# Optimization experiments

Measured on AMD Instinct MI355X. Metric: run time of the kernel, lower is better.

The kernel has to match this reference:

```python
import jax, jax.numpy as jnp
import numpy as np

RATE = 2
KSIZE = 3          # patch size for similarity
KERNEL = 2 * RATE  # patch size for alpha scatter (4)
BN_EPS = 1e-5


def _extract_patches(x, k, s):
    """Mirror of GuidedCxtAtten.extract_patches: reflect-pad then unfold.
    x: [B,C,H,W] -> [B,Ho,Wo,C,k,k] with Ho=H//s, Wo=W//s."""
    left = (k - s + 1) // 2
    right = (k - s) // 2
    xp = jnp.pad(x, ((0, 0), (0, 0), (left, right), (left, right)), mode='reflect')
    Hp, Wp = xp.shape[2], xp.shape[3]
    Ho = (Hp - k) // s + 1
    Wo = (Wp - k) // s + 1
    ii = (jnp.arange(Ho) * s)[:, None] + jnp.arange(k)[None, :]   # [Ho,k]
    jj = (jnp.arange(Wo) * s)[:, None] + jnp.arange(k)[None, :]   # [Wo,k]
    p = xp[:, :, ii[:, :, None, None], jj[None, None, :, :]]      # [B,C,Ho,k,Wo,k]
    return p.transpose(0, 2, 4, 1, 3, 5)                          # [B,Ho,Wo,C,k,k]


def setup_inputs() -> dict:
    key = jax.random.key(0)
    ks = jax.random.split(key, 5)
    B, Cg, Ca, H, W = 4, 256, 128, 128, 128
    f = jax.random.normal(ks[0], (B, Cg, H, W), dtype=jnp.float32)
    alpha = jax.random.normal(ks[1], (B, Ca, H, W), dtype=jnp.float32)
    unknown = (jax.random.uniform(ks[2], (B, 1, H, W)) > 0.5).astype(jnp.float32)
    # guidance_conv: 1x1, Cg -> Cg//2, xavier-ish
    gc_w = jax.random.normal(ks[3], (Cg // 2, Cg), dtype=jnp.float32) * np.sqrt(2.0 / (Cg + Cg // 2))
    gc_b = jnp.zeros((Cg // 2,), dtype=jnp.float32)
    # W[0]: 1x1 conv Ca->Ca no bias; W[1]: BN with gamma=0.001, beta=0 per init
    w_w = jax.random.normal(ks[4], (Ca, Ca), dtype=jnp.float32) * np.sqrt(1.0 / Ca)
    bn_gamma = jnp.full((Ca,), 0.001, dtype=jnp.float32)
    bn_beta = jnp.zeros((Ca,), dtype=jnp.float32)
    return {"f": f, "alpha": alpha, "unknown": unknown, "gc_w": gc_w, "gc_b": gc_b,
            "w_w": w_w, "bn_gamma": bn_gamma, "bn_beta": bn_beta}


def _forward(f, alpha, unknown, gc_w, gc_b, w_w, bn_gamma, bn_beta):
    # guidance 1x1 conv
    fg = jnp.einsum('oi,bihw->bohw', gc_w, f) + gc_b[None, :, None, None]
    B, _, H, W = fg.shape
    Ca = alpha.shape[1]
    Hs, Ws = H // RATE, W // RATE
    L = Hs * Ws

    # alpha patches [B,L,Ca,4,4] (kernel=2*rate, stride=rate)
    alpha_w = _extract_patches(alpha, KERNEL, RATE).reshape(B, L, Ca, KERNEL, KERNEL)

    # nearest downsample by rate (torch nearest with scale 1/2 == strided pick)
    f_ds = fg[:, :, ::RATE, ::RATE]                # [B,Cg/2,Hs,Ws]
    unk_ds = unknown[:, :, ::RATE, ::RATE]         # [B,1,Hs,Ws]

    # similarity filter patches [B,L,C,3,3]
    w = _extract_patches(f_ds, KSIZE, 1).reshape(B, L, -1, KSIZE, KSIZE)

    # known/unknown softmax scales [B,2]
    u_mean = unk_ds.mean(axis=(2, 3))              # [B,1]
    k_mean = 1.0 - u_mean
    su = jnp.clip(jnp.sqrt(u_mean / k_mean), 0.1, 10.0)
    sk = jnp.clip(jnp.sqrt(k_mean / u_mean), 0.1, 10.0)
    softmax_scale = jnp.concatenate([su, sk], axis=1)

    # patch-mean of unknown mask -> binary patch mask [B,L]
    m = _extract_patches(unk_ds, KSIZE, 1).reshape(B, L, -1).mean(axis=2)
    mm = (m > 0.0).astype(fg.dtype)

    # l2-normalize filters per patch, then correlate against all positions.
    # Conv of reflect-padded f_ds with stride-1 3x3 patch filters == inner
    # product of normalized patches with the raw patches (same extraction).
    norm = jnp.sqrt(jnp.sum(w * w, axis=(2, 3, 4), keepdims=True))
    w_normed = w / jnp.maximum(norm, 1e-4)
    scores = jnp.einsum('bqcij,bpcij->bqp', w_normed, w)   # [B,L(q=patch),L(p=pos)]

    # known/unknown scaling per source patch q
    gate = jnp.where(mm > 0.0, su, sk)                      # [B,L]
    scores = scores * gate[:, :, None]

    # self-match suppression only for unknown patches (diagonal q == p)
    diag = jnp.arange(L)
    scores = scores.at[:, diag, diag].add(-10000.0 * mm)

    attn = jax.nn.softmax(scores, axis=1)                   # softmax over patches q

    # offsets (argmax patch per position, relative to center)
    idx = jnp.argmax(attn, axis=1)                          # [B,L]
    offsets = jnp.stack([idx // Ws, idx % Ws], axis=1).reshape(B, 2, Hs, Ws)
    offsets = offsets - jnp.array([Hs // 2, Ws // 2]).reshape(1, 2, 1, 1)

    # scatter alpha patches with attention weights: per-sample conv_transpose2d
    attn_map = attn.reshape(B, L, Hs, Ws)

    def ct(yi, wc):  # yi [L,Hs,Ws], wc [L,Ca,4,4]
        rhs = jnp.flip(wc, (2, 3)).transpose(1, 0, 2, 3)    # [Ca,L,4,4]
        pad = KERNEL - 1 - 1                                # torch padding=1
        out = jax.lax.conv_general_dilated(
            yi[None], rhs, window_strides=(1, 1),
            padding=[(pad, pad), (pad, pad)], lhs_dilation=(RATE, RATE),
            dimension_numbers=('NCHW', 'OIHW', 'NCHW'))
        return out[0]

    y = jax.vmap(ct)(attn_map, alpha_w) / 4.0               # [B,Ca,H,W]

    # W: 1x1 conv (no bias) + BatchNorm2d (training-mode batch stats)
    yw = jnp.einsum('oi,bihw->bohw', w_w, y)
    mean = yw.mean(axis=(0, 2, 3))
    var = yw.var(axis=(0, 2, 3))
    yn = (yw - mean[None, :, None, None]) * jax.lax.rsqrt(var + BN_EPS)[None, :, None, None]
    yn = yn * bn_gamma[None, :, None, None] + bn_beta[None, :, None, None]

    return yn + alpha, offsets, softmax_scale


def reference(f, alpha, unknown, gc_w, gc_b, w_w, bn_gamma, bn_beta):
    return _forward(f, alpha, unknown, gc_w, gc_b, w_w, bn_gamma, bn_beta)
```

## Files before the change

### kernel.cpp

```cpp
#include <hip/hip_runtime.h>
#include <math.h>

#define B 4
#define CG 256
#define CM 128
#define CA 128
#define H 128
#define W_ 128
#define HS 64
#define WS 64
#define L 4096
#define D1 1152
#define D2 2048
#define NPIX 65536
#define NT1 36
#define NT2 128

#define STP_F 8388608UL
#define WF_F  4718592UL
#define ZB_F  4194304UL
#define SLOT_F (STP_F + WF_F + ZB_F)

typedef unsigned short u16;
typedef __attribute__((ext_vector_type(8))) short short8v;
typedef __attribute__((ext_vector_type(4))) unsigned short u16x4;
typedef __attribute__((ext_vector_type(4))) float f32x4;

__device__ __forceinline__ float bf2f(u16 x) {
    union { unsigned int u; float f; } v; v.u = ((unsigned int)x) << 16; return v.f;
}
__device__ __forceinline__ u16 f2bf(float x) {
    union { float f; unsigned int u; } v; v.f = x;
    unsigned int r = (v.u + 0x7FFFu + ((v.u >> 16) & 1u)) >> 16;
    return (u16)r;
}
__device__ __forceinline__ void gll16(const void* g, void* l) {
    __builtin_amdgcn_global_load_lds((const __attribute__((address_space(1))) void*)g,
                                     (__attribute__((address_space(3))) void*)l, 16, 0, 0);
}
__device__ __forceinline__ int refl(int i, int n) {
    return i < 0 ? -i : (i >= n ? 2 * n - 2 - i : i);
}
__device__ __forceinline__ int swz(int row, int fq) {
    return row * 32 + ((fq ^ ((row >> 1) & 3)) * 8);
}

__device__ __forceinline__ void stage32(const u16* __restrict__ mat, int rowTile,
                                        int kt, u16* lds, int wid, int lane) {
#pragma unroll
    for (int c = 0; c < 2; ++c) {
        int off = c * 8192 + wid * 1024 + lane * 16;
        int row = off >> 6;
        int cb  = off & 63;
        const u16* g = mat + (size_t)(rowTile + row) * L + kt * 32
                     + ((cb ^ (((row >> 1) & 3) << 4)) >> 1);
        gll16(g, (char*)lds + c * 8192 + wid * 1024);
    }
}
__device__ __forceinline__ short8v rdfrag32(const u16* lds, int r, int fq) {
    return *(const short8v*)((const char*)lds + r * 64 + ((fq * 16) ^ (((r >> 1) & 3) << 4)));
}

__global__ __launch_bounds__(256) void k_conv_ds(const float* __restrict__ f,
                                                 const float* __restrict__ gw,
                                                 const float* __restrict__ gb,
                                                 float* __restrict__ fds,
                                                 float* __restrict__ ssq) {
    __shared__ float sf[CG * 64];
    __shared__ float part[4][64];
    int t = threadIdx.x;
    int hs = blockIdx.x, b = blockIdx.y;
    const float* fb = f + (size_t)b * CG * H * W_ + (2 * hs) * W_;
    for (int idx = t; idx < CG * 64; idx += 256) {
        int ci = idx >> 6, ws = idx & 63;
        sf[idx] = fb[(size_t)ci * H * W_ + 2 * ws];
    }
    __syncthreads();
    int ws = t & 63;
    int wave = __builtin_amdgcn_readfirstlane(t >> 6);
    const float* gwp = gw + (size_t)(wave * 32) * CG;
    float acc[32];
#pragma unroll
    for (int r = 0; r < 32; ++r) acc[r] = gb[wave * 32 + r];
    for (int ci = 0; ci < CG; ++ci) {
        float fv = sf[ci * 64 + ws];
#pragma unroll
        for (int r = 0; r < 32; ++r) acc[r] += gwp[r * CG + ci] * fv;
    }
    float sq = 0.f;
#pragma unroll
    for (int r = 0; r < 32; ++r) {
        int co = wave * 32 + r;
        fds[(((size_t)b * CM + co) * HS + hs) * WS + ws] = acc[r];
        sq += acc[r] * acc[r];
    }
    part[wave][ws] = sq;
    __syncthreads();
    if (t < 64)
        ssq[((size_t)b * HS + hs) * WS + t] =
            part[0][t] + part[1][t] + part[2][t] + part[3][t];
}

__global__ __launch_bounds__(256) void k_scale(const float* __restrict__ unk,
                                               float* __restrict__ suk,
                                               float* __restrict__ out2) {
    int b = blockIdx.x, t = threadIdx.x;
    __shared__ float red[256];
    float s = 0.f;
    for (int i = t; i < L; i += 256) {
        int hs = i >> 6, ws = i & 63;
        s += unk[(size_t)b * H * W_ + (2 * hs) * W_ + 2 * ws];
    }
    red[t] = s;
    __syncthreads();
    for (int o = 128; o > 0; o >>= 1) {
        if (t < o) red[t] += red[t + o];
        __syncthreads();
    }
    if (t == 0) {
        float u = red[0] / (float)L;
        float k = 1.0f - u;
        float su = sqrtf(u / k); su = fminf(fmaxf(su, 0.1f), 10.0f);
        float sk = sqrtf(k / u); sk = fminf(fmaxf(sk, 0.1f), 10.0f);
        suk[b * 2] = su; suk[b * 2 + 1] = sk;
        out2[b * 2] = su; out2[b * 2 + 1] = sk;
    }
}

__global__ __launch_bounds__(64) void k_gate(const float* __restrict__ unk,
                                             const float* __restrict__ ssq,
                                             const float* __restrict__ suk,
                                             float* __restrict__ g,
                                             float* __restrict__ dg) {
    int ws = threadIdx.x, hs = blockIdx.x, b = blockIdx.y;
    float sm = 0.f, sq = 0.f;
    for (int di = -1; di <= 1; ++di) {
        int rh = refl(hs + di, HS);
        for (int dj = -1; dj <= 1; ++dj) {
            int rw = refl(ws + dj, WS);
            sm += unk[(size_t)b * H * W_ + (2 * rh) * W_ + 2 * rw];
            sq += ssq[((size_t)b * HS + rh) * WS + rw];
        }
    }
    float mm   = (sm > 0.0f) ? 1.0f : 0.0f;
    float norm = sqrtf(sq);
    float gate = (mm > 0.0f) ? suk[2 * b] : suk[2 * b + 1];
    int q = hs * WS + ws;
    g[(size_t)b * L + q]  = gate / fmaxf(norm, 1e-4f);
    dg[(size_t)b * L + q] = -10000.0f * mm;
}

__global__ __launch_bounds__(256) void k_buildW(const float* __restrict__ fds,
                                                float* __restrict__ base, int b0) {
    int bz = blockIdx.z;
    int b  = b0 + bz;
    float* S   = base + (size_t)bz * SLOT_F;
    float* Wf  = S + STP_F;
    u16*   Whi = (u16*)(S + STP_F + WF_F);
    int ws = threadIdx.x;
    int c  = blockIdx.y * 4 + threadIdx.y;
    int hs = blockIdx.x;
    int q = hs * WS + ws;
    size_t bo = (size_t)q * D1 + c * 9;
    const float* src = fds + ((size_t)b * CM + c) * HS * WS;
#pragma unroll
    for (int i = 0; i < 3; ++i) {
        int rh = refl(hs + i - 1, HS);
#pragma unroll
        for (int j = 0; j < 3; ++j) {
            int rw = refl(ws + j - 1, WS);
            float v = src[rh * WS + rw];
            Wf[bo + i * 3 + j]  = v;
            Whi[bo + i * 3 + j] = f2bf(v);
        }
    }
}

__global__ __launch_bounds__(256) void k_gemm1(float* __restrict__ base,
                                               const float* __restrict__ g0,
                                               const float* __restrict__ dg0,
                                               int b0) {
    __shared__ u16 sA[3][128 * 32], sB[3][128 * 32];
    int bz = blockIdx.z;
    float* S = base + (size_t)bz * SLOT_F;
    u16* STP = (u16*)S;
    const u16* Whi = (const u16*)(S + STP_F + WF_F);
    const float* g  = g0  + (size_t)(b0 + bz) * L;
    const float* dg = dg0 + (size_t)(b0 + bz) * L;

    int tid = threadIdx.x;
    int wv = tid >> 6, lane = tid & 63;
    int t0 = blockIdx.x, I = 0;
    while (t0 >= 32 - I) { t0 -= 32 - I; ++I; }
    int J = I + t0;
    int pTile = I * 128, qTile = J * 128;
    int wp = (wv >> 1) * 64, wq = (wv & 1) * 64;
    int r0 = wv * 32;
    int lrow = lane >> 2;
    int csw = ((lane & 3) ^ ((lrow >> 1) & 3)) * 8;
    int fr = lane & 15, fq = lane >> 4;

    const u16* gArow = Whi + (size_t)(pTile + r0 + lrow) * D1 + csw;
    const u16* gBrow = Whi + (size_t)(qTile + r0 + lrow) * D1 + csw;

#define G1STAGE(kt, bf) do { \
    gll16(gArow + (kt) * 32, &sA[bf][r0 * 32]); \
    gll16(gArow + (kt) * 32 + (size_t)16 * D1, &sA[bf][(r0 + 16) * 32]); \
    gll16(gBrow + (kt) * 32, &sB[bf][r0 * 32]); \
    gll16(gBrow + (kt) * 32 + (size_t)16 * D1, &sB[bf][(r0 + 16) * 32]); } while (0)

    f32x4 acc[4][4];
#pragma unroll
    for (int mi = 0; mi < 4; ++mi)
#pragma unroll
        for (int ni = 0; ni < 4; ++ni)
#pragma unroll
            for (int r = 0; r < 4; ++r) acc[mi][ni][r] = 0.f;

    G1STAGE(0, 0);
    G1STAGE(1, 1);
    asm volatile("s_waitcnt vmcnt(4)" ::: "memory");
    __builtin_amdgcn_s_barrier();
    __builtin_amdgcn_sched_barrier(0);

    for (int t = 0; t < NT1; ++t) {
        int cur = t % 3;
        short8v ah[4], bh[4];
#pragma unroll
        for (int i = 0; i < 4; ++i) {
            ah[i] = *(const short8v*)&sA[cur][swz(wp + i * 16 + fr, fq)];
            bh[i] = *(const short8v*)&sB[cur][swz(wq + i * 16 + fr, fq)];
        }
        __builtin_amdgcn_s_setprio(1);
#pragma unroll
        for (int mi = 0; mi < 2; ++mi)
#pragma unroll
            for (int ni = 0; ni < 4; ++ni)
                acc[mi][ni] = __builtin_amdgcn_mfma_f32_16x16x32_bf16(ah[mi], bh[ni], acc[mi][ni], 0, 0, 0);
        __builtin_amdgcn_s_setprio(0);
        int kt2 = (t + 2 < NT1) ? (t + 2) : 0;
        G1STAGE(kt2, (t + 2) % 3);
        asm volatile("s_waitcnt vmcnt(4)" ::: "memory");
        __builtin_amdgcn_sched_barrier(0);
        __builtin_amdgcn_s_setprio(1);
#pragma unroll
        for (int mi = 2; mi < 4; ++mi)
#pragma unroll
            for (int ni = 0; ni < 4; ++ni)
                acc[mi][ni] = __builtin_amdgcn_mfma_f32_16x16x32_bf16(ah[mi], bh[ni], acc[mi][ni], 0, 0, 0);
        __builtin_amdgcn_s_setprio(0);
        __builtin_amdgcn_s_barrier();
        __builtin_amdgcn_sched_barrier(0);
    }
#undef G1STAGE

#pragma unroll
    for (int ni = 0; ni < 4; ++ni) {
        int qq = qTile + wq + ni * 16 + fr;
        float gq = g[qq];
        float dq = dg[qq];
#pragma unroll
        for (int mi = 0; mi < 4; ++mi) {
            int pB = pTile + wp + mi * 16 + fq * 4;
#pragma unroll
            for (int r = 0; r < 4; ++r) {
                int p = pB + r;
                float v = acc[mi][ni][r] * gq;
                if (p == qq) v += dq;
                STP[(size_t)p * L + qq] = f2bf(v);
            }
        }
    }
    if (I != J) {
#pragma unroll
        for (int mi = 0; mi < 4; ++mi) {
            int p0 = pTile + wp + mi * 16 + fq * 4;
            float gp0 = g[p0], gp1 = g[p0 + 1], gp2 = g[p0 + 2], gp3 = g[p0 + 3];
#pragma unroll
            for (int ni = 0; ni < 4; ++ni) {
                int qq = qTile + wq + ni * 16 + fr;
                u16x4 mv;
                mv[0] = f2bf(acc[mi][ni][0] * gp0);
                mv[1] = f2bf(acc[mi][ni][1] * gp1);
                mv[2] = f2bf(acc[mi][ni][2] * gp2);
                mv[3] = f2bf(acc[mi][ni][3] * gp3);
                *(u16x4*)(STP + (size_t)qq * L + p0) = mv;
            }
        }
    }
}

__global__ __launch_bounds__(256) void k_softmax(float* __restrict__ base,
                                                 const float* __restrict__ g0,
                                                 const float* __restrict__ dg0,
                                                 float* __restrict__ out1, int b0) {
    __shared__ float buf[L];
    __shared__ float wmax[4], wsum[4], cred[4];
    __shared__ int candList[128];
    __shared__ int candCount;
    int bz = blockIdx.y;
    int b  = b0 + bz;
    float* S = base + (size_t)bz * SLOT_F;
    u16* STP = (u16*)S;
    const float* Wf = S + STP_F;
    const float* g  = g0  + (size_t)b * L;
    const float* dg = dg0 + (size_t)b * L;

    int p = blockIdx.x, t = threadIdx.x;
    int lane = t & 63, wv = t >> 6;
    u16* rowp = STP + (size_t)p * L;

    if (t == 0) candCount = 0;
    float mx = -3.4e38f;
    for (int i = t; i < L / 8; i += 256) {
        short8v v8 = ((const short8v*)rowp)[i];
#pragma unroll
        for (int j = 0; j < 8; ++j) {
            float v = bf2f((u16)v8[j]);
            buf[i * 8 + j] = v;
            mx = fmaxf(mx, v);
        }
    }
#pragma unroll
    for (int o = 32; o > 0; o >>= 1) mx = fmaxf(mx, __shfl_xor(mx, o));
    if (lane == 0) wmax[wv] = mx;
    __syncthreads();
    float M = fmaxf(fmaxf(wmax[0], wmax[1]), fmaxf(wmax[2], wmax[3]));
    float cth = M - (fabsf(M) * 0.0625f + 1e-5f);

    float s = 0.f;
    for (int i = t; i < L; i += 256) {
        float v = buf[i];
        if (v >= cth) {
            int ix = atomicAdd(&candCount, 1);
            if (ix < 128) candList[ix] = i;
        }
        float e = __expf(v - M);
        buf[i] = e;
        s += e;
    }
#pragma unroll
    for (int o = 32; o > 0; o >>= 1) s += __shfl_xor(s, o);
    if (lane == 0) wsum[wv] = s;
    __syncthreads();
    float inv = 1.0f / (wsum[0] + wsum[1] + wsum[2] + wsum[3]);

    for (int i = t; i < L / 8; i += 256) {
        short8v o8;
#pragma unroll
        for (int j = 0; j < 8; ++j) o8[j] = (short)f2bf(buf[i * 8 + j] * inv);
        ((short8v*)rowp)[i] = o8;
    }

    int nc = candCount; if (nc > 128) nc = 128;
    int bestI;
    if (nc == 1) {
        bestI = candList[0];
    } else {
        float bestE = -3.4e38f; bestI = L;
        const float* wp_ = Wf + (size_t)p * D1;
        for (int k = 0; k < nc; ++k) {
            int cand = candList[k];
            const float* wc = Wf + (size_t)cand * D1;
            float part = 0.f;
            for (int j = t; j < D1; j += 256) part += wp_[j] * wc[j];
#pragma unroll
            for (int o = 32; o > 0; o >>= 1) part += __shfl_xor(part, o);
            if (lane == 0) cred[wv] = part;
            __syncthreads();
            float e1 = (cred[0] + cred[1] + cred[2] + cred[3]) * g[cand]
                     + (p == cand ? dg[cand] : 0.f);
            if (e1 > bestE || (e1 == bestE && cand < bestI)) { bestE = e1; bestI = cand; }
            __syncthreads();
        }
    }
    if (t == 0) {
        out1[(size_t)(b * 2 + 0) * L + p] = (float)(bestI / WS - 32);
        out1[(size_t)(b * 2 + 1) * L + p] = (float)(bestI % WS - 32);
    }
}

__global__ __launch_bounds__(256) void k_buildA(const float* __restrict__ alpha,
                                                float* __restrict__ base, int b0) {
    int bz = blockIdx.z;
    int b  = b0 + bz;
    u16* At = (u16*)(base + (size_t)bz * SLOT_F + STP_F);
    int q = blockIdx.x * 256 + threadIdx.x;
    int n = blockIdx.y;
    int hs = q >> 6, ws = q & 63;
    int c = n >> 4, ki = (n >> 2) & 3, kj = n & 3;
    int rh = refl(2 * hs + ki - 1, H);
    int rw = refl(2 * ws + kj - 1, W_);
    At[(size_t)n * L + q] = f2bf(alpha[((size_t)b * CA + c) * H * W_ + rh * W_ + rw]);
}

__global__ __launch_bounds__(512, 2) void k_gemm2(float* __restrict__ base) {
    __shared__ u16 smem[65536];
    int bz = blockIdx.z;
    float* S = base + (size_t)bz * SLOT_F;
    const u16* P  = (const u16*)S;
    const u16* At = (const u16*)(S + STP_F);
    u16* Z        = (u16*)(S + STP_F + WF_F);

    int tid = threadIdx.x;
    int wid = tid >> 6, lane = tid & 63;
    int wm = wid >> 2, wn = wid & 3;
    int pTile = blockIdx.x * 256, nTile = blockIdx.y * 256;
    int fr = lane & 15, fq = lane >> 4;

    f32x4 acc[8][4];
#pragma unroll
    for (int m = 0; m < 8; ++m)
#pragma unroll
        for (int n = 0; n < 4; ++n)
#pragma unroll
            for (int r = 0; r < 4; ++r) acc[m][n][r] = 0.f;

    stage32(P,  pTile, 0, smem,         wid, lane);
    stage32(At, nTile, 0, smem + 8192,  wid, lane);
    stage32(P,  pTile, 1, smem + 16384, wid, lane);
    stage32(At, nTile, 1, smem + 24576, wid, lane);
    stage32(P,  pTile, 2, smem + 32768, wid, lane);
    stage32(At, nTile, 2, smem + 40960, wid, lane);
    asm volatile("s_waitcnt vmcnt(8)" ::: "memory");
    __builtin_amdgcn_s_barrier();
    __builtin_amdgcn_sched_barrier(0);

    for (int t = 0; t < NT2; ++t) {
        const u16* Ab = smem + (t & 3) * 16384;
        const u16* Bb = Ab + 8192;
        short8v a[8], b[4];
#pragma unroll
        for (int n = 0; n < 4; ++n) b[n] = rdfrag32(Bb, wn * 64 + n * 16 + fr, fq);
#pragma unroll
        for (int m = 0; m < 4; ++m) a[m] = rdfrag32(Ab, wm * 128 + m * 16 + fr, fq);
        __builtin_amdgcn_s_setprio(1);
#pragma unroll
        for (int m = 0; m < 2; ++m)
#pragma unroll
            for (int n = 0; n < 4; ++n)
                acc[m][n] = __builtin_amdgcn_mfma_f32_16x16x32_bf16(a[m], b[n], acc[m][n], 0, 0, 0);
        __builtin_amdgcn_s_setprio(0);
#pragma unroll
        for (int m = 4; m < 8; ++m) a[m] = rdfrag32(Ab, wm * 128 + m * 16 + fr, fq);
        __builtin_amdgcn_s_setprio(1);
#pragma unroll
        for (int m = 2; m < 6; ++m)
#pragma unroll
            for (int n = 0; n < 4; ++n)
                acc[m][n] = __builtin_amdgcn_mfma_f32_16x16x32_bf16(a[m], b[n], acc[m][n], 0, 0, 0);
        __builtin_amdgcn_s_setprio(0);
        int kt3 = (t + 3 < NT2) ? (t + 3) : 0;
        u16* d3 = smem + ((t + 3) & 3) * 16384;
        stage32(P,  pTile, kt3, d3,        wid, lane);
        stage32(At, nTile, kt3, d3 + 8192, wid, lane);
        asm volatile("s_waitcnt vmcnt(8)" ::: "memory");
        __builtin_amdgcn_sched_barrier(0);
        __builtin_amdgcn_s_setprio(1);
#pragma unroll
        for (int m = 6; m < 8; ++m)
#pragma unroll
            for (int n = 0; n < 4; ++n)
                acc[m][n] = __builtin_amdgcn_mfma_f32_16x16x32_bf16(a[m], b[n], acc[m][n], 0, 0, 0);
        __builtin_amdgcn_s_setprio(0);
        __builtin_amdgcn_s_barrier();
        __builtin_amdgcn_sched_barrier(0);
    }

#pragma unroll
    for (int m = 0; m < 8; ++m)
#pragma unroll
        for (int n = 0; n < 4; ++n) {
            int nn = nTile + wn * 64 + n * 16 + fr;
#pragma unroll
            for (int r = 0; r < 4; ++r) {
                int pp = pTile + wm * 128 + m * 16 + fq * 4 + r;
                Z[(size_t)pp * D2 + nn] = f2bf(acc[m][n][r]);
            }
        }
}

__global__ __launch_bounds__(256) void k_gather(float* __restrict__ base,
                                                u16* __restrict__ yt, int b0) {
    int bz = blockIdx.z;
    int b  = b0 + bz;
    const u16* Z = (const u16*)(base + (size_t)bz * SLOT_F + STP_F + WF_F);
    int c  = threadIdx.x & 127;
    int pl = threadIdx.x >> 7;
    int w  = blockIdx.x * 2 + pl;
    int h  = blockIdx.y;
    float s = 0.f;
#pragma unroll
    for (int ki = 0; ki < 4; ++ki) {
        int num = h + 1 - ki;
        if (num < 0 || (num & 1)) continue;
        int hs = num >> 1;
        if (hs >= HS) continue;
#pragma unroll
        for (int kj = 0; kj < 4; ++kj) {
            int numw = w + 1 - kj;
            if (numw < 0 || (numw & 1)) continue;
            int wsd = numw >> 1;
            if (wsd >= WS) continue;
            s += bf2f(Z[(size_t)(hs * WS + wsd) * D2 + c * 16 + ki * 4 + kj]);
        }
    }
    int pix = h * W_ + w;
    int cs = c ^ ((pix & 7) << 3);
    yt[((size_t)b * 16384 + pix) * 128 + cs] = f2bf(0.25f * s);
}

__global__ __launch_bounds__(256) void k_cvtww(const float* __restrict__ ww,
                                               u16* __restrict__ wwbf) {
    int i = blockIdx.x * 256 + threadIdx.x;
    int o = i >> 7, c = i & 127;
    wwbf[o * 128 + (c ^ ((o & 7) << 3))] = f2bf(ww[i]);
}

__global__ __launch_bounds__(256) void k_ywgemm(const u16* __restrict__ wwbf,
                                                const u16* __restrict__ yt,
                                                float* __restrict__ yw) {
    __shared__ u16 sA[128 * 128], sB[128 * 128];
    int tid = threadIdx.x;
    int wv = tid >> 6, lane = tid & 63;
    int nTile = blockIdx.x * 128;
    int wp = (wv >> 1) * 64, wn = (wv & 1) * 64;
    int fr = lane & 15, fq = lane >> 4;

    const u16* gB = yt + (size_t)nTile * 128;
#pragma unroll
    for (int i = 0; i < 8; ++i) {
        int o = (i * 4 + wv) * 512;
        gll16(wwbf + o + lane * 8, &sA[o]);
        gll16(gB + o + lane * 8, &sB[o]);
    }
    __syncthreads();

    f32x4 acc[4][4];
#pragma unroll
    for (int mi = 0; mi < 4; ++mi)
#pragma unroll
        for (int ni = 0; ni < 4; ++ni)
#pragma unroll
            for (int r = 0; r < 4; ++r) acc[mi][ni][r] = 0.f;

#pragma unroll
    for (int ks = 0; ks < 4; ++ks) {
        int k0 = ks * 32 + fq * 8;
        short8v a[4], bb[4];
#pragma unroll
        for (int i = 0; i < 4; ++i) {
            int ra = wp + i * 16 + fr;
            a[i] = *(const short8v*)&sA[ra * 128 + (k0 ^ ((ra & 7) << 3))];
            int rb = wn + i * 16 + fr;
            bb[i] = *(const short8v*)&sB[rb * 128 + (k0 ^ ((rb & 7) << 3))];
        }
#pragma unroll
        for (int mi = 0; mi < 4; ++mi)
#pragma unroll
            for (int ni = 0; ni < 4; ++ni)
                acc[mi][ni] = __builtin_amdgcn_mfma_f32_16x16x32_bf16(a[mi], bb[ni], acc[mi][ni], 0, 0, 0);
    }

#pragma unroll
    for (int mi = 0; mi < 4; ++mi)
#pragma unroll
        for (int ni = 0; ni < 4; ++ni) {
            int gp = nTile + wn + ni * 16 + fr;
#pragma unroll
            for (int r = 0; r < 4; ++r) {
                int o = wp + mi * 16 + fq * 4 + r;
                yw[(size_t)o * NPIX + gp] = acc[mi][ni][r];
            }
        }
}

__global__ __launch_bounds__(256) void k_stats(const float* __restrict__ yw,
                                               float* __restrict__ meanvar) {
    int o = blockIdx.x, t = threadIdx.x;
    __shared__ float rs[256], rq[256];
    float s = 0.f, q = 0.f;
    const float* p = yw + (size_t)o * NPIX;
    for (int i = t; i < NPIX; i += 256) {
        float v = p[i];
        s += v;
        q += v * v;
    }
    rs[t] = s; rq[t] = q;
    __syncthreads();
    for (int off = 128; off > 0; off >>= 1) {
        if (t < off) { rs[t] += rs[t + off]; rq[t] += rq[t + off]; }
        __syncthreads();
    }
    if (t == 0) {
        float n = (float)NPIX;
        float mean = rs[0] / n;
        float var  = rq[0] / n - mean * mean;
        meanvar[o] = mean;
        meanvar[CA + o] = var;
    }
}

__global__ __launch_bounds__(256) void k_final(const float* __restrict__ yw,
                                               const float* __restrict__ meanvar,
                                               const float* __restrict__ gamma,
                                               const float* __restrict__ beta,
                                               const float* __restrict__ alpha,
                                               float* __restrict__ out0) {
    size_t i = ((size_t)blockIdx.x * 256 + threadIdx.x) * 4;
    int c = (int)((i >> 14) & 127);
    int b = (int)(i >> 21);
    int pix = (int)(i & 16383);
    float4 v = *(const float4*)(yw + (size_t)c * NPIX + b * 16384 + pix);
    float4 a = *(const float4*)(alpha + i);
    float mean = meanvar[c];
    float var  = meanvar[CA + c];
    float sc   = rsqrtf(var + 1e-5f) * gamma[c];
    float bt   = beta[c];
    float4 r;
    r.x = (v.x - mean) * sc + bt + a.x;
    r.y = (v.y - mean) * sc + bt + a.y;
    r.z = (v.z - mean) * sc + bt + a.z;
    r.w = (v.w - mean) * sc + bt + a.w;
    *(float4*)(out0 + i) = r;
}

extern "C" void kernel_launch(void* const* d_in, const int* in_sizes, int n_in,
                              void* d_out, int out_size, void* d_ws, size_t ws_size,
                              hipStream_t stream) {
    (void)in_sizes; (void)n_in; (void)out_size;
    const float* f     = (const float*)d_in[0];
    const float* alpha = (const float*)d_in[1];
    const float* unk   = (const float*)d_in[2];
    const float* gw    = (const float*)d_in[3];
    const float* gb    = (const float*)d_in[4];
    const float* ww    = (const float*)d_in[5];
    const float* gamma = (const float*)d_in[6];
    const float* beta  = (const float*)d_in[7];

    float* out0 = (float*)d_out;
    float* out1 = out0 + (size_t)B * CA * H * W_;
    float* out2 = out1 + (size_t)B * 2 * HS * WS;

    float* wsf = (float*)d_ws;
    size_t off = 0;
    float* fds     = wsf + off; off += (size_t)B * CM * HS * WS;
    float* ssq     = wsf + off; off += (size_t)B * HS * WS;
    float* gbuf    = wsf + off; off += (size_t)B * L;
    float* dgbuf   = wsf + off; off += (size_t)B * L;
    float* suk     = wsf + off; off += 64;
    float* ytF     = wsf + off; off += (size_t)NPIX * 128 / 2;
    float* wwbfF   = wsf + off; off += 8192;
    float* meanvar = wsf + off; off += 256;
    float* base    = wsf + off;

    const size_t PRE_F = off;
    int nb = (ws_size >= (PRE_F + 4 * SLOT_F) * sizeof(float)) ? 4 : 2;

    float* yw   = base;
    u16*   yt   = (u16*)ytF;
    u16*   wwbf = (u16*)wwbfF;

    k_cvtww<<<64, 256, 0, stream>>>(ww, wwbf);
    k_conv_ds<<<dim3(64, 4), 256, 0, stream>>>(f, gw, gb, fds, ssq);
    k_scale<<<4, 256, 0, stream>>>(unk, suk, out2);
    k_gate<<<dim3(64, 4), 64, 0, stream>>>(unk, ssq, suk, gbuf, dgbuf);

    for (int b0 = 0; b0 < B; b0 += nb) {
        k_buildW<<<dim3(64, 32, nb), dim3(64, 4), 0, stream>>>(fds, base, b0);
        k_gemm1<<<dim3(528, 1, nb), 256, 0, stream>>>(base, gbuf, dgbuf, b0);
        k_softmax<<<dim3(4096, nb), 256, 0, stream>>>(base, gbuf, dgbuf, out1, b0);
        k_buildA<<<dim3(16, 2048, nb), 256, 0, stream>>>(alpha, base, b0);
        k_gemm2<<<dim3(16, 8, nb), 512, 0, stream>>>(base);
        k_gather<<<dim3(64, 128, nb), 256, 0, stream>>>(base, yt, b0);
    }

    k_ywgemm<<<512, 256, 0, stream>>>(wwbf, yt, yw);
    k_stats<<<128, 256, 0, stream>>>(yw, meanvar);
    k_final<<<8192, 256, 0, stream>>>(yw, meanvar, gamma, beta, alpha, out0);
}
```

Measured before the change: 846.5 us.

## Double-buffer MFMA fragments in registers to overlap LDS reads with compute

Restructures the second GEMM's main loop so fragments for the next K tile are read from LDS into a second register set while MFMAs consume the current set, with the loop unrolled by two. Global-to-LDS staging addresses are precomputed once instead of recomputed per stage. The aim is to hide LDS read latency behind matrix instructions. It roughly doubles fragment register usage, which may raise register pressure or cause spills under the existing launch bounds.

Measured after the change: 843.8 us. About the same (-0.3%).

```diff
diff --git a/kernel.cpp b/kernel.cpp
--- a/kernel.cpp
+++ b/kernel.cpp
@@ -44,21 +44,8 @@
 __device__ __forceinline__ int swz(int row, int fq) {
     return row * 32 + ((fq ^ ((row >> 1) & 3)) * 8);
 }
-
-__device__ __forceinline__ void stage32(const u16* __restrict__ mat, int rowTile,
-                                        int kt, u16* lds, int wid, int lane) {
-#pragma unroll
-    for (int c = 0; c < 2; ++c) {
-        int off = c * 8192 + wid * 1024 + lane * 16;
-        int row = off >> 6;
-        int cb  = off & 63;
-        const u16* g = mat + (size_t)(rowTile + row) * L + kt * 32
-                     + ((cb ^ (((row >> 1) & 3) << 4)) >> 1);
-        gll16(g, (char*)lds + c * 8192 + wid * 1024);
-    }
-}
-__device__ __forceinline__ short8v rdfrag32(const u16* lds, int r, int fq) {
-    return *(const short8v*)((const char*)lds + r * 64 + ((fq * 16) ^ (((r >> 1) & 3) << 4)));
+__device__ __forceinline__ short8v rdfrag32(const char* lds, int r, int fq) {
+    return *(const short8v*)(lds + r * 64 + ((fq * 16) ^ (((r >> 1) & 3) << 4)));
 }
 
 __global__ __launch_bounds__(256) void k_conv_ds(const float* __restrict__ f,
@@ -396,6 +383,7 @@
 
 __global__ __launch_bounds__(512, 2) void k_gemm2(float* __restrict__ base) {
     __shared__ u16 smem[65536];
+    char* sm = (char*)smem;
     int bz = blockIdx.z;
     float* S = base + (size_t)bz * SLOT_F;
     const u16* P  = (const u16*)S;
@@ -408,6 +396,49 @@
     int pTile = blockIdx.x * 256, nTile = blockIdx.y * 256;
     int fr = lane & 15, fq = lane >> 4;
 
+    int off0 = wid * 1024 + lane * 16;
+    int row0 = off0 >> 6, cb0 = off0 & 63;
+    int off1 = off0 + 8192;
+    int row1 = off1 >> 6, cb1 = off1 & 63;
+    const u16* pA0 = P  + (size_t)(pTile + row0) * L + ((cb0 ^ (((row0 >> 1) & 3) << 4)) >> 1);
+    const u16* pA1 = P  + (size_t)(pTile + row1) * L + ((cb1 ^ (((row1 >> 1) & 3) << 4)) >> 1);
+    const u16* pB0 = At + (size_t)(nTile + row0) * L + ((cb0 ^ (((row0 >> 1) & 3) << 4)) >> 1);
+    const u16* pB1 = At + (size_t)(nTile + row1) * L + ((cb1 ^ (((row1 >> 1) & 3) << 4)) >> 1);
+
+#define STG2(kt, bi) do { \
+    char* d = sm + (bi) * 32768 + wid * 1024; \
+    gll16(pA0 + (size_t)(kt) * 32, d); \
+    gll16(pA1 + (size_t)(kt) * 32, d + 8192); \
+    gll16(pB0 + (size_t)(kt) * 32, d + 16384); \
+    gll16(pB1 + (size_t)(kt) * 32, d + 24576); } while (0)
+
+#define PRELOAD2(fa, fb, bi) do { \
+    const char* Ab_ = sm + (bi) * 32768; \
+    const char* Bb_ = Ab_ + 16384; \
+    _Pragma("unroll") for (int n = 0; n < 4; ++n) fb[n] = rdfrag32(Bb_, wn * 64 + n * 16 + fr, fq); \
+    _Pragma("unroll") for (int m = 0; m < 8; ++m) fa[m] = rdfrag32(Ab_, wm * 128 + m * 16 + fr, fq); } while (0)
+
+#define PHASE2(t, ca, cb, na, nb_) do { \
+    const char* Abn = sm + (((t) + 1) & 3) * 32768; \
+    const char* Bbn = Abn + 16384; \
+    _Pragma("unroll") for (int n = 0; n < 4; ++n) nb_[n] = rdfrag32(Bbn, wn * 64 + n * 16 + fr, fq); \
+    __builtin_amdgcn_s_setprio(1); \
+    _Pragma("unroll") for (int m = 0; m < 4; ++m) \
+        _Pragma("unroll") for (int n = 0; n < 4; ++n) \
+            acc[m][n] = __builtin_amdgcn_mfma_f32_16x16x32_bf16(ca[m], cb[n], acc[m][n], 0, 0, 0); \
+    __builtin_amdgcn_s_setprio(0); \
+    _Pragma("unroll") for (int m = 0; m < 8; ++m) na[m] = rdfrag32(Abn, wm * 128 + m * 16 + fr, fq); \
+    STG2(((t) + 3 < NT2) ? (t) + 3 : 0, ((t) + 3) & 3); \
+    asm volatile("s_waitcnt vmcnt(4)" ::: "memory"); \
+    __builtin_amdgcn_s_setprio(1); \
+    _Pragma("unroll") for (int m = 4; m < 8; ++m) \
+        _Pragma("unroll") for (int n = 0; n < 4; ++n) \
+            acc[m][n] = __builtin_amdgcn_mfma_f32_16x16x32_bf16(ca[m], cb[n], acc[m][n], 0, 0, 0); \
+    __builtin_amdgcn_s_setprio(0); \
+    asm volatile("s_waitcnt lgkmcnt(0)" ::: "memory"); \
+    __builtin_amdgcn_s_barrier(); \
+    __builtin_amdgcn_sched_barrier(0); } while (0)
+
     f32x4 acc[8][4];
 #pragma unroll
     for (int m = 0; m < 8; ++m)
@@ -416,56 +447,25 @@
 #pragma unroll
             for (int r = 0; r < 4; ++r) acc[m][n][r] = 0.f;
 
-    stage32(P,  pTile, 0, smem,         wid, lane);
-    stage32(At, nTile, 0, smem + 8192,  wid, lane);
-    stage32(P,  pTile, 1, smem + 16384, wid, lane);
-    stage32(At, nTile, 1, smem + 24576, wid, lane);
-    stage32(P,  pTile, 2, smem + 32768, wid, lane);
-    stage32(At, nTile, 2, smem + 40960, wid, lane);
-    asm volatile("s_waitcnt vmcnt(8)" ::: "memory");
+    STG2(0, 0);
+    STG2(1, 1);
+    STG2(2, 2);
+    asm volatile("s_waitcnt vmcnt(4)" ::: "memory");
     __builtin_amdgcn_s_barrier();
     __builtin_amdgcn_sched_barrier(0);
 
-    for (int t = 0; t < NT2; ++t) {
-        const u16* Ab = smem + (t & 3) * 16384;
-        const u16* Bb = Ab + 8192;
-        short8v a[8], b[4];
-#pragma unroll
-        for (int n = 0; n < 4; ++n) b[n] = rdfrag32(Bb, wn * 64 + n * 16 + fr, fq);
-#pragma unroll
-        for (int m = 0; m < 4; ++m) a[m] = rdfrag32(Ab, wm * 128 + m * 16 + fr, fq);
-        __builtin_amdgcn_s_setprio(1);
-#pragma unroll
-        for (int m = 0; m < 2; ++m)
-#pragma unroll
-            for (int n = 0; n < 4; ++n)
-                acc[m][n] = __builtin_amdgcn_mfma_f32_16x16x32_bf16(a[m], b[n], acc[m][n], 0, 0, 0);
-        __builtin_amdgcn_s_setprio(0);
-#pragma unroll
-        for (int m = 4; m < 8; ++m) a[m] = rdfrag32(Ab, wm * 128 + m * 16 + fr, fq);
-        __builtin_amdgcn_s_setprio(1);
-#pragma unroll
-        for (int m = 2; m < 6; ++m)
-#pragma unroll
-            for (int n = 0; n < 4; ++n)
-                acc[m][n] = __builtin_amdgcn_mfma_f32_16x16x32_bf16(a[m], b[n], acc[m][n], 0, 0, 0);
-        __builtin_amdgcn_s_setprio(0);
-        int kt3 = (t + 3 < NT2) ? (t + 3) : 0;
-        u16* d3 = smem + ((t + 3) & 3) * 16384;
-        stage32(P,  pTile, kt3, d3,        wid, lane);
-        stage32(At, nTile, kt3, d3 + 8192, wid, lane);
-        asm volatile("s_waitcnt vmcnt(8)" ::: "memory");
-        __builtin_amdgcn_sched_barrier(0);
-        __builtin_amdgcn_s_setprio(1);
-#pragma unroll
-        for (int m = 6; m < 8; ++m)
-#pragma unroll
-            for (int n = 0; n < 4; ++n)
-                acc[m][n] = __builtin_amdgcn_mfma_f32_16x16x32_bf16(a[m], b[n], acc[m][n], 0, 0, 0);
-        __builtin_amdgcn_s_setprio(0);
-        __builtin_amdgcn_s_barrier();
-        __builtin_amdgcn_sched_barrier(0);
-    }
+    short8v fa0[8], fb0[4], fa1[8], fb1[4];
+    PRELOAD2(fa0, fb0, 0);
+    asm volatile("s_waitcnt lgkmcnt(0)" ::: "memory");
+    __builtin_amdgcn_sched_barrier(0);
+
+    for (int t = 0; t < NT2; t += 2) {
+        PHASE2(t,     fa0, fb0, fa1, fb1);
+        PHASE2(t + 1, fa1, fb1, fa0, fb0);
+    }
+#undef PHASE2
+#undef PRELOAD2
+#undef STG2
 
 #pragma unroll
     for (int m = 0; m < 8; ++m)
```
